# Optimization experiments

Measured on AMD Instinct MI355X. Metric: run time of the kernel, lower is better.

## Reference

```python
import jax, jax.numpy as jnp
import numpy as np

D_MODEL = 1024
N_HEADS = 16
D_KV = 64
B, S = 2, 2048


def setup_inputs() -> dict:
    key = jax.random.key(0)
    ks = jax.random.split(key, 7)
    scale = 1.0 / np.sqrt(D_MODEL)
    return {
        "query": jax.random.normal(ks[0], (B, S, D_MODEL), jnp.float32),
        "key": jax.random.normal(ks[1], (B, S, D_MODEL), jnp.float32),
        "value": jax.random.normal(ks[2], (B, S, D_MODEL), jnp.float32),
        "mask": jnp.zeros((B, 1, 1, S), jnp.float32),
        "Wq": jax.random.normal(ks[3], (D_MODEL, N_HEADS * D_KV), jnp.float32) * scale,
        "Wk": jax.random.normal(ks[4], (D_MODEL, N_HEADS * D_KV), jnp.float32) * scale,
        "Wv": jax.random.normal(ks[5], (D_MODEL, N_HEADS * D_KV), jnp.float32) * scale,
        "Wo": jax.random.normal(ks[6], (N_HEADS * D_KV, D_MODEL), jnp.float32) * scale,
    }


def _split_heads(x):
    b, s, _ = x.shape
    return x.reshape(b, s, N_HEADS, D_KV).transpose(0, 2, 1, 3)  # [B,H,S,Dk]


def reference(query, key, value, mask, Wq, Wk, Wv, Wo):
    q = _split_heads(query @ Wq)
    k = _split_heads(key @ Wk)
    v = _split_heads(value @ Wv)
    scores = jnp.einsum("bhqd,bhkd->bhqk", q, k) / jnp.sqrt(
        jnp.asarray(D_KV, scores_dtype := q.dtype)
    )
    scores = scores + mask
    attn = jax.nn.softmax(scores, axis=-1)  # dropout_rate=0 -> identity
    ctx = jnp.einsum("bhqk,bhkd->bhqd", attn, v)
    ctx = ctx.transpose(0, 2, 1, 3).reshape(query.shape[0], -1, N_HEADS * D_KV)
    hidden = ctx @ Wo
    return hidden
```

## Files before the change

kernel.cpp:

```cpp
#include <hip/hip_runtime.h>
#include <hip/hip_bf16.h>
#include <stdint.h>

typedef __bf16 bf16;
typedef __bf16 bf16x8 __attribute__((ext_vector_type(8)));
typedef __bf16 bf16x4 __attribute__((ext_vector_type(4)));
typedef float  f32x4  __attribute__((ext_vector_type(4)));
typedef float  f32x16 __attribute__((ext_vector_type(16)));

#define S_LEN  2048
#define NH     16
#define DKV    64
#define DMODEL 1024
#define LOG2E  1.4426950408889634f

__device__ __forceinline__ void async_load16(const void* g, void* l) {
  __builtin_amdgcn_global_load_lds(
      (const __attribute__((address_space(1))) uint32_t*)(uintptr_t)g,
      (__attribute__((address_space(3))) uint32_t*)(uintptr_t)l,
      16, 0, 0);
}

__global__ void transpose_w(const float* __restrict__ W0, const float* __restrict__ W1,
                            const float* __restrict__ W2, const float* __restrict__ W3,
                            bf16* __restrict__ T0, bf16* __restrict__ T1,
                            bf16* __restrict__ T2, bf16* __restrict__ T3)
{
  int z = blockIdx.z;
  const float* W = (z == 0) ? W0 : (z == 1) ? W1 : (z == 2) ? W2 : W3;
  bf16* T = (z == 0) ? T0 : (z == 1) ? T1 : (z == 2) ? T2 : T3;
  __shared__ float tile[32][33];
  int n0 = blockIdx.x * 32, k0 = blockIdx.y * 32;
  int tx = threadIdx.x, ty = threadIdx.y;
  for (int i = 0; i < 32; i += 8)
    tile[ty + i][tx] = W[(size_t)(k0 + ty + i) * DMODEL + n0 + tx];
  __syncthreads();
  for (int i = 0; i < 32; i += 8)
    T[(size_t)(n0 + ty + i) * DMODEL + k0 + tx] = (bf16)tile[tx][ty + i];
}

__global__ __launch_bounds__(256) void gemm_qkv(
    const float* __restrict__ Aq, const float* __restrict__ Ak, const float* __restrict__ Av,
    const bf16* __restrict__ Bq, const bf16* __restrict__ Bk, const bf16* __restrict__ Bv,
    bf16* __restrict__ Cq, bf16* __restrict__ Ck, bf16* __restrict__ Cv)
{
  __shared__ __align__(16) char smem[24576];
  bf16* As = (bf16*)smem;
  bf16* Bs = (bf16*)smem + 64 * 64;
  bf16* Ls = (bf16*)smem;

  const int z = blockIdx.z;
  const float* A = (z == 0) ? Aq : (z == 1) ? Ak : Av;
  const bf16* Bt = (z == 0) ? Bq : (z == 1) ? Bk : Bv;
  bf16* C        = (z == 0) ? Cq : (z == 1) ? Ck : Cv;

  const int m0 = blockIdx.x * 64;
  const int n0 = blockIdx.y * 128;
  const int tid = threadIdx.x;
  const int lane = tid & 63;
  const int wave = tid >> 6;
  const int wm = (wave >> 1) * 32;
  const int wn = (wave & 1) * 64;
  const int row = lane & 15;
  const int quad = lane >> 4;

  f32x4 acc[2][4];
  for (int i = 0; i < 2; ++i)
    for (int j = 0; j < 4; ++j) acc[i][j] = (f32x4){0.f, 0.f, 0.f, 0.f};

  const int arc = tid & 7;
  const int arr = tid >> 3;
  const float* A0p = A + (size_t)(m0 + arr) * DMODEL + arc * 8;
  const float* A1p = A + (size_t)(m0 + 32 + arr) * DMODEL + arc * 8;

  f32x4 av0[2], av1[2];
  av0[0] = *(const f32x4*)(A0p);
  av1[0] = *(const f32x4*)(A0p + 4);
  av0[1] = *(const f32x4*)(A1p);
  av1[1] = *(const f32x4*)(A1p + 4);

  for (int kt = 0; kt < 16; ++kt) {
    const int kk = kt << 6;
    __syncthreads();
    for (int j = 0; j < 4; ++j) {
      int base = j * 256 + wave * 64;
      int idx = base + lane;
      int r = idx >> 3;
      int cc = (idx & 7) ^ (r & 7);
      async_load16(Bt + (size_t)(n0 + r) * DMODEL + kk + cc * 8,
                   (char*)Bs + (size_t)base * 16);
    }
    for (int u = 0; u < 2; ++u) {
      bf16x8 o;
      for (int w = 0; w < 4; ++w) { o[w] = (bf16)av0[u][w]; o[w + 4] = (bf16)av1[u][w]; }
      int r = u * 32 + arr;
      *(bf16x8*)(As + r * 64 + ((arc ^ (r & 7)) << 3)) = o;
    }
    __syncthreads();
    if (kt < 15) {
      const int kn = kk + 64;
      av0[0] = *(const f32x4*)(A0p + kn);
      av1[0] = *(const f32x4*)(A0p + kn + 4);
      av0[1] = *(const f32x4*)(A1p + kn);
      av1[1] = *(const f32x4*)(A1p + kn + 4);
    }
    for (int ks = 0; ks < 2; ++ks) {
      bf16x8 af[2], bfr[4];
      for (int i = 0; i < 2; ++i) {
        int rr = wm + i * 16 + row;
        af[i] = *(const bf16x8*)(As + rr * 64 + (((quad + ks * 4) ^ (rr & 7)) << 3));
      }
      for (int j = 0; j < 4; ++j) {
        int rr = wn + j * 16 + row;
        bfr[j] = *(const bf16x8*)(Bs + rr * 64 + (((quad + ks * 4) ^ (rr & 7)) << 3));
      }
      for (int i = 0; i < 2; ++i)
        for (int j = 0; j < 4; ++j)
          acc[i][j] = __builtin_amdgcn_mfma_f32_16x16x32_bf16(af[i], bfr[j], acc[i][j], 0, 0, 0);
    }
  }

  if (z != 2) {
    const int bq = m0 >> 11;
    __syncthreads();
    for (int i = 0; i < 2; ++i)
      for (int j = 0; j < 4; ++j)
        for (int r = 0; r < 4; ++r)
          Ls[(wm + i * 16 + quad * 4 + r) * 132 + wn + j * 16 + row] = (bf16)acc[i][j][r];
    __syncthreads();
    for (int u = 0; u < 4; ++u) {
      int cc = u * 256 + tid;
      int rloc = cc >> 4, c8 = (cc & 15) * 8;
      int s = (m0 + rloc) & 2047;
      int gn = n0 + c8;
      int h = gn >> 6, d = gn & 63;
      bf16x8 val = *(const bf16x8*)(Ls + rloc * 132 + c8);
      *(bf16x8*)(C + (((size_t)(bq * NH + h)) * S_LEN + s) * DKV + d) = val;
    }
  } else {
    for (int i = 0; i < 2; ++i)
      for (int j = 0; j < 4; ++j) {
        int gm = m0 + wm + i * 16 + quad * 4;
        int gn = n0 + wn + j * 16 + row;
        int b = gm >> 11, s = gm & 2047;
        int h = gn >> 6,  d = gn & 63;
        int bh = b * NH + h;
        int tile = s >> 6, kb = (s & 63) >> 2;
        bf16x4 t;
        for (int r = 0; r < 4; ++r) t[r] = (bf16)acc[i][j][r];
        *(bf16x4*)(C + ((((size_t)bh * 32 + tile) * 16 + kb) * 64 + d) * 4) = t;
      }
  }
}

__global__ __launch_bounds__(256, 4) void attn_kernel(
    const bf16* __restrict__ Qh, const bf16* __restrict__ Kh, const bf16* __restrict__ Vperm,
    const float* __restrict__ mask, bf16* __restrict__ Opart, float* __restrict__ Lpart)
{
  __shared__ __align__(16) bf16 Ks[64 * 64];
  __shared__ __align__(16) bf16 Vts[64 * 64];
  __shared__ __align__(16) float masks2[64];

  const int bh = blockIdx.x;
  const int b = bh >> 4;
  const int q0 = blockIdx.y * 128;
  const int zh = blockIdx.z;
  const int tid = threadIdx.x;
  const int lane = tid & 63;
  const int wave = tid >> 6;
  const int ln = lane & 31;
  const int hi = lane >> 5;
  const float SC2 = 0.125f * LOG2E;

  const int qg = q0 + wave * 32 + ln;
  bf16x8 qf[4];
  {
    const bf16* qrow = Qh + ((size_t)bh * S_LEN + qg) * DKV;
    for (int c = 0; c < 4; ++c)
      qf[c] = *(const bf16x8*)(qrow + c * 16 + hi * 8);
  }

  f32x16 O[2];
  for (int nb = 0; nb < 2; ++nb)
    for (int i = 0; i < 16; ++i) O[nb][i] = 0.f;
  float lsum = 0.f;

  for (int it = 0; it < 16; ++it) {
    const int kv0 = zh * 1024 + it * 64;
    __syncthreads();
    const bf16* vtile = Vperm + ((size_t)bh * 32 + (kv0 >> 6)) * 4096;
    for (int j = 0; j < 2; ++j) {
      int base = j * 256 + wave * 64;
      int idx = base + lane;
      int r = idx >> 3;
      int cc = (idx & 7) ^ (r & 7);
      async_load16(Kh + ((size_t)bh * S_LEN + kv0 + r) * DKV + cc * 8,
                   (char*)Ks + (size_t)base * 16);
      async_load16(vtile + (size_t)idx * 8,
                   (char*)Vts + (size_t)base * 16);
    }
    if (tid < 64) masks2[tid] = mask[b * S_LEN + kv0 + tid] * LOG2E;
    __syncthreads();

    f32x16 Sm[2];
    for (int i = 0; i < 16; ++i) { Sm[0][i] = 0.f; Sm[1][i] = 0.f; }
    for (int c = 0; c < 4; ++c) {
      bf16x8 k0 = *(const bf16x8*)(Ks + ln * 64        + (((2 * c + hi) ^ (ln & 7)) << 3));
      bf16x8 k1 = *(const bf16x8*)(Ks + (32 + ln) * 64 + (((2 * c + hi) ^ (ln & 7)) << 3));
      Sm[0] = __builtin_amdgcn_mfma_f32_32x32x16_bf16(k0, qf[c], Sm[0], 0, 0, 0);
      Sm[1] = __builtin_amdgcn_mfma_f32_32x32x16_bf16(k1, qf[c], Sm[1], 0, 0, 0);
    }

    for (int cg = 0; cg < 4; ++cg) {
      int mb = cg >> 1, g = cg & 1;
      int koff = 32 * mb + 16 * g + 4 * hi;
      f32x4 mklo = *(const f32x4*)(masks2 + koff);
      f32x4 mkhi = *(const f32x4*)(masks2 + koff + 8);
      bf16x8 ap;
      float ls0 = 0.f;
      for (int u = 0; u < 4; ++u) {
        float p = __builtin_amdgcn_exp2f(Sm[mb][g * 8 + u] * SC2 + mklo[u]);
        ls0 += p; ap[u] = (bf16)p;
      }
      for (int u = 0; u < 4; ++u) {
        float p = __builtin_amdgcn_exp2f(Sm[mb][g * 8 + 4 + u] * SC2 + mkhi[u]);
        ls0 += p; ap[4 + u] = (bf16)p;
      }
      lsum += ls0;
      int kb0 = hi + 4 * g + 8 * mb;
      for (int nb = 0; nb < 2; ++nb) {
        int d = nb * 32 + ln;
        bf16x4 lo = *(const bf16x4*)(Vts + ((size_t)kb0 * 64 + d) * 4);
        bf16x4 hv = *(const bf16x4*)(Vts + ((size_t)(kb0 + 2) * 64 + d) * 4);
        bf16x8 bv;
        for (int u = 0; u < 4; ++u) { bv[u] = lo[u]; bv[u + 4] = hv[u]; }
        O[nb] = __builtin_amdgcn_mfma_f32_32x32x16_bf16(ap, bv, O[nb], 0, 0, 0);
      }
    }
  }

  float lt = lsum + __shfl_xor(lsum, 32, 64);
  if (lane < 32)
    Lpart[((size_t)zh * 32 + bh) * S_LEN + q0 + wave * 32 + ln] = lt;

  bf16* ob = Opart + (((size_t)zh * 32 + bh) * S_LEN) * DKV;
  for (int g = 0; g < 4; ++g)
    for (int nb = 0; nb < 2; ++nb)
      for (int j = 0; j < 4; ++j) {
        int qrow = q0 + wave * 32 + j + 8 * g + 4 * hi;
        ob[(size_t)qrow * DKV + nb * 32 + ln] = (bf16)O[nb][g * 4 + j];
      }
}

__global__ __launch_bounds__(256) void gemm_out(
    const bf16* __restrict__ Opart, const float* __restrict__ Lpart,
    const bf16* __restrict__ Wot, float* __restrict__ Cout)
{
  __shared__ __align__(16) bf16 As[32 * 64];
  __shared__ __align__(16) bf16 Bs[128 * 64];
  __shared__ float rinv[NH * 32];

  const int m0 = blockIdx.x * 32;
  const int n0 = blockIdx.y * 128;
  const int tid = threadIdx.x;
  const int lane = tid & 63;
  const int wave = tid >> 6;
  const int wm = (wave >> 1) * 16;
  const int wn = (wave & 1) * 64;
  const int row = lane & 15;
  const int quad = lane >> 4;
  const int b = m0 >> 11;
  const int s0 = m0 & 2047;

  for (int u = 0; u < 2; ++u) {
    int idx = u * 256 + tid;
    int h = idx >> 5, r = idx & 31;
    float l = Lpart[((size_t)(b * NH + h)) * S_LEN + s0 + r]
            + Lpart[((size_t)(32 + b * NH + h)) * S_LEN + s0 + r];
    rinv[idx] = 1.0f / l;
  }

  f32x4 acc[4];
  for (int j = 0; j < 4; ++j) acc[j] = (f32x4){0.f, 0.f, 0.f, 0.f};

  const int arc = tid & 7;
  const int arr = tid >> 3;
  const bf16* O0p = Opart + ((size_t)(b * NH) * S_LEN + s0 + arr) * DKV + arc * 8;
  const bf16* O1p = Opart + ((size_t)(32 + b * NH) * S_LEN + s0 + arr) * DKV + arc * 8;
  const size_t HSTEP = (size_t)S_LEN * DKV;

  bf16x8 h0 = *(const bf16x8*)(O0p);
  bf16x8 h1 = *(const bf16x8*)(O1p);

  for (int kt = 0; kt < 16; ++kt) {
    __syncthreads();
    for (int j = 0; j < 4; ++j) {
      int base = j * 256 + wave * 64;
      int idx = base + lane;
      int r = idx >> 3;
      int cc = (idx & 7) ^ (r & 7);
      async_load16(Wot + (size_t)(n0 + r) * DMODEL + kt * 64 + cc * 8,
                   (char*)Bs + (size_t)base * 16);
    }
    {
      float rv = rinv[kt * 32 + arr];
      bf16x8 o;
      for (int w = 0; w < 8; ++w)
        o[w] = (bf16)(((float)h0[w] + (float)h1[w]) * rv);
      *(bf16x8*)(As + arr * 64 + ((arc ^ (arr & 7)) << 3)) = o;
    }
    __syncthreads();
    if (kt < 15) {
      h0 = *(const bf16x8*)(O0p + (size_t)(kt + 1) * HSTEP);
      h1 = *(const bf16x8*)(O1p + (size_t)(kt + 1) * HSTEP);
    }
    for (int ks = 0; ks < 2; ++ks) {
      bf16x8 af, bfr[4];
      {
        int rr = wm + row;
        af = *(const bf16x8*)(As + rr * 64 + (((quad + ks * 4) ^ (rr & 7)) << 3));
      }
      for (int j = 0; j < 4; ++j) {
        int rr = wn + j * 16 + row;
        bfr[j] = *(const bf16x8*)(Bs + rr * 64 + (((quad + ks * 4) ^ (rr & 7)) << 3));
      }
      for (int j = 0; j < 4; ++j)
        acc[j] = __builtin_amdgcn_mfma_f32_16x16x32_bf16(af, bfr[j], acc[j], 0, 0, 0);
    }
  }

  for (int j = 0; j < 4; ++j)
    for (int r = 0; r < 4; ++r) {
      int gm = m0 + wm + quad * 4 + r;
      int gn = n0 + wn + j * 16 + row;
      Cout[(size_t)gm * DMODEL + gn] = acc[j][r];
    }
}

extern "C" void kernel_launch(void* const* d_in, const int* in_sizes, int n_in,
                              void* d_out, int out_size, void* d_ws, size_t ws_size,
                              hipStream_t stream)
{
  const float* query = (const float*)d_in[0];
  const float* key_  = (const float*)d_in[1];
  const float* value = (const float*)d_in[2];
  const float* mask  = (const float*)d_in[3];
  const float* Wq = (const float*)d_in[4];
  const float* Wk = (const float*)d_in[5];
  const float* Wv = (const float*)d_in[6];
  const float* Wo = (const float*)d_in[7];

  char* ws = (char*)d_ws;
  const size_t MB = (size_t)1 << 20;
  bf16* qh    = (bf16*)(ws + 0 * MB);
  bf16* kh    = (bf16*)(ws + 8 * MB);
  bf16* vperm = (bf16*)(ws + 16 * MB);
  bf16* wot   = (bf16*)(ws + 24 * MB);
  bf16* Opart = (bf16*)(ws + 26 * MB);
  bf16* wqt   = (bf16*)(ws + 26 * MB);
  bf16* wkt   = (bf16*)(ws + 28 * MB);
  bf16* wvt   = (bf16*)(ws + 30 * MB);
  float* Lpart = (float*)(ws + 58 * MB);

  transpose_w<<<dim3(32, 32, 4), dim3(32, 8), 0, stream>>>(Wq, Wk, Wv, Wo, wqt, wkt, wvt, wot);
  gemm_qkv<<<dim3(64, 8, 3), 256, 0, stream>>>(query, key_, value, wqt, wkt, wvt,
                                               qh, kh, vperm);
  attn_kernel<<<dim3(32, 16, 2), 256, 0, stream>>>(qh, kh, vperm, mask, Opart, Lpart);
  gemm_out<<<dim3(128, 8), 256, 0, stream>>>(Opart, Lpart, wot, (float*)d_out);
}
```

Before: 224.4 us.

## Double-buffer LDS tiles with async prefetch in QKV, attention and output kernels

Adds a second LDS buffer for the async-loaded B/K/V tiles in all three main kernels and issues the next tile's global-to-LDS loads before computing on the current one. The __syncthreads pairs are replaced with manual s_waitcnt vmcnt counts, sched_barrier fences and raw s_barrier. The aim is to hide global load latency behind MFMA work. In exchange the kernels use more LDS, which may lower occupancy in the attention kernel, and correctness now depends on hand-counted vmcnt values matching the number of outstanding loads.

Measured after the change: 215.5 us. -4.0%, faster.

```diff
diff --git a/kernel.cpp b/kernel.cpp
--- a/kernel.cpp
+++ b/kernel.cpp
@@ -13,6 +13,11 @@
 #define DKV    64
 #define DMODEL 1024
 #define LOG2E  1.4426950408889634f
+
+#define SBAR()       __builtin_amdgcn_s_barrier()
+#define SFENCE()     __builtin_amdgcn_sched_barrier(0)
+#define WAIT_VM(N)   asm volatile("s_waitcnt vmcnt(" #N ")" ::: "memory")
+#define WAIT_LGKM0() asm volatile("s_waitcnt lgkmcnt(0)" ::: "memory")
 
 __device__ __forceinline__ void async_load16(const void* g, void* l) {
   __builtin_amdgcn_global_load_lds(
@@ -44,10 +49,11 @@
     const bf16* __restrict__ Bq, const bf16* __restrict__ Bk, const bf16* __restrict__ Bv,
     bf16* __restrict__ Cq, bf16* __restrict__ Ck, bf16* __restrict__ Cv)
 {
-  __shared__ __align__(16) char smem[24576];
-  bf16* As = (bf16*)smem;
-  bf16* Bs = (bf16*)smem + 64 * 64;
-  bf16* Ls = (bf16*)smem;
+  __shared__ __align__(16) char smem[40960];
+  bf16* As  = (bf16*)smem;
+  bf16* Bs0 = (bf16*)(smem + 8192);
+  bf16* Bs1 = (bf16*)(smem + 8192 + 16384);
+  bf16* Ls  = (bf16*)smem;
 
   const int z = blockIdx.z;
   const float* A = (z == 0) ? Aq : (z == 1) ? Ak : Av;
@@ -73,37 +79,49 @@
   const float* A0p = A + (size_t)(m0 + arr) * DMODEL + arc * 8;
   const float* A1p = A + (size_t)(m0 + 32 + arr) * DMODEL + arc * 8;
 
-  f32x4 av0[2], av1[2];
-  av0[0] = *(const f32x4*)(A0p);
-  av1[0] = *(const f32x4*)(A0p + 4);
-  av0[1] = *(const f32x4*)(A1p);
-  av1[1] = *(const f32x4*)(A1p + 4);
-
-  for (int kt = 0; kt < 16; ++kt) {
+  auto stageB = [&](int kt, bf16* Bsel) {
     const int kk = kt << 6;
-    __syncthreads();
     for (int j = 0; j < 4; ++j) {
       int base = j * 256 + wave * 64;
       int idx = base + lane;
       int r = idx >> 3;
       int cc = (idx & 7) ^ (r & 7);
       async_load16(Bt + (size_t)(n0 + r) * DMODEL + kk + cc * 8,
-                   (char*)Bs + (size_t)base * 16);
-    }
+                   (char*)Bsel + (size_t)base * 16);
+    }
+  };
+
+  f32x4 av0[2], av1[2];
+  av0[0] = *(const f32x4*)(A0p);
+  av1[0] = *(const f32x4*)(A0p + 4);
+  av0[1] = *(const f32x4*)(A1p);
+  av1[1] = *(const f32x4*)(A1p + 4);
+
+  stageB(0, Bs0);
+
+  for (int kt = 0; kt < 16; ++kt) {
+    bf16* Bcur = (kt & 1) ? Bs1 : Bs0;
+    bf16* Bnxt = (kt & 1) ? Bs0 : Bs1;
+    if (kt < 15) stageB(kt + 1, Bnxt);
     for (int u = 0; u < 2; ++u) {
       bf16x8 o;
       for (int w = 0; w < 4; ++w) { o[w] = (bf16)av0[u][w]; o[w + 4] = (bf16)av1[u][w]; }
       int r = u * 32 + arr;
       *(bf16x8*)(As + r * 64 + ((arc ^ (r & 7)) << 3)) = o;
     }
-    __syncthreads();
     if (kt < 15) {
-      const int kn = kk + 64;
+      const int kn = (kt + 1) << 6;
       av0[0] = *(const f32x4*)(A0p + kn);
       av1[0] = *(const f32x4*)(A0p + kn + 4);
       av0[1] = *(const f32x4*)(A1p + kn);
       av1[1] = *(const f32x4*)(A1p + kn + 4);
     }
+    SFENCE();
+    if (kt < 15) { WAIT_VM(8); }
+    else         { WAIT_VM(0); }
+    WAIT_LGKM0();
+    SBAR();
+    SFENCE();
     for (int ks = 0; ks < 2; ++ks) {
       bf16x8 af[2], bfr[4];
       for (int i = 0; i < 2; ++i) {
@@ -112,12 +130,14 @@
       }
       for (int j = 0; j < 4; ++j) {
         int rr = wn + j * 16 + row;
-        bfr[j] = *(const bf16x8*)(Bs + rr * 64 + (((quad + ks * 4) ^ (rr & 7)) << 3));
+        bfr[j] = *(const bf16x8*)(Bcur + rr * 64 + (((quad + ks * 4) ^ (rr & 7)) << 3));
       }
       for (int i = 0; i < 2; ++i)
         for (int j = 0; j < 4; ++j)
           acc[i][j] = __builtin_amdgcn_mfma_f32_16x16x32_bf16(af[i], bfr[j], acc[i][j], 0, 0, 0);
     }
+    SFENCE();
+    SBAR();
   }
 
   if (z != 2) {
@@ -157,9 +177,9 @@
     const bf16* __restrict__ Qh, const bf16* __restrict__ Kh, const bf16* __restrict__ Vperm,
     const float* __restrict__ mask, bf16* __restrict__ Opart, float* __restrict__ Lpart)
 {
-  __shared__ __align__(16) bf16 Ks[64 * 64];
-  __shared__ __align__(16) bf16 Vts[64 * 64];
-  __shared__ __align__(16) float masks2[64];
+  __shared__ __align__(16) bf16 Ks[2][64 * 64];
+  __shared__ __align__(16) bf16 Vts[2][64 * 64];
+  __shared__ __align__(16) float masks2[2][64];
 
   const int bh = blockIdx.x;
   const int b = bh >> 4;
@@ -180,14 +200,10 @@
       qf[c] = *(const bf16x8*)(qrow + c * 16 + hi * 8);
   }
 
-  f32x16 O[2];
-  for (int nb = 0; nb < 2; ++nb)
-    for (int i = 0; i < 16; ++i) O[nb][i] = 0.f;
-  float lsum = 0.f;
-
-  for (int it = 0; it < 16; ++it) {
+  auto stage = [&](int it, int buf) {
     const int kv0 = zh * 1024 + it * 64;
-    __syncthreads();
+    float mval = 0.f;
+    if (tid < 64) mval = mask[b * S_LEN + kv0 + tid];
     const bf16* vtile = Vperm + ((size_t)bh * 32 + (kv0 >> 6)) * 4096;
     for (int j = 0; j < 2; ++j) {
       int base = j * 256 + wave * 64;
@@ -195,18 +211,35 @@
       int r = idx >> 3;
       int cc = (idx & 7) ^ (r & 7);
       async_load16(Kh + ((size_t)bh * S_LEN + kv0 + r) * DKV + cc * 8,
-                   (char*)Ks + (size_t)base * 16);
+                   (char*)Ks[buf] + (size_t)base * 16);
       async_load16(vtile + (size_t)idx * 8,
-                   (char*)Vts + (size_t)base * 16);
-    }
-    if (tid < 64) masks2[tid] = mask[b * S_LEN + kv0 + tid] * LOG2E;
-    __syncthreads();
+                   (char*)Vts[buf] + (size_t)base * 16);
+    }
+    if (tid < 64) masks2[buf][tid] = mval * LOG2E;
+  };
+
+  f32x16 O[2];
+  for (int nb = 0; nb < 2; ++nb)
+    for (int i = 0; i < 16; ++i) O[nb][i] = 0.f;
+  float lsum = 0.f;
+
+  stage(0, 0);
+
+  for (int it = 0; it < 16; ++it) {
+    const int cur = it & 1;
+    if (it < 15) stage(it + 1, cur ^ 1);
+    SFENCE();
+    if (it < 15) { WAIT_VM(4); }
+    else         { WAIT_VM(0); }
+    WAIT_LGKM0();
+    SBAR();
+    SFENCE();
 
     f32x16 Sm[2];
     for (int i = 0; i < 16; ++i) { Sm[0][i] = 0.f; Sm[1][i] = 0.f; }
     for (int c = 0; c < 4; ++c) {
-      bf16x8 k0 = *(const bf16x8*)(Ks + ln * 64        + (((2 * c + hi) ^ (ln & 7)) << 3));
-      bf16x8 k1 = *(const bf16x8*)(Ks + (32 + ln) * 64 + (((2 * c + hi) ^ (ln & 7)) << 3));
+      bf16x8 k0 = *(const bf16x8*)(Ks[cur] + ln * 64        + (((2 * c + hi) ^ (ln & 7)) << 3));
+      bf16x8 k1 = *(const bf16x8*)(Ks[cur] + (32 + ln) * 64 + (((2 * c + hi) ^ (ln & 7)) << 3));
       Sm[0] = __builtin_amdgcn_mfma_f32_32x32x16_bf16(k0, qf[c], Sm[0], 0, 0, 0);
       Sm[1] = __builtin_amdgcn_mfma_f32_32x32x16_bf16(k1, qf[c], Sm[1], 0, 0, 0);
     }
@@ -214,8 +247,8 @@
     for (int cg = 0; cg < 4; ++cg) {
       int mb = cg >> 1, g = cg & 1;
       int koff = 32 * mb + 16 * g + 4 * hi;
-      f32x4 mklo = *(const f32x4*)(masks2 + koff);
-      f32x4 mkhi = *(const f32x4*)(masks2 + koff + 8);
+      f32x4 mklo = *(const f32x4*)(&masks2[cur][koff]);
+      f32x4 mkhi = *(const f32x4*)(&masks2[cur][koff + 8]);
       bf16x8 ap;
       float ls0 = 0.f;
       for (int u = 0; u < 4; ++u) {
@@ -230,13 +263,15 @@
       int kb0 = hi + 4 * g + 8 * mb;
       for (int nb = 0; nb < 2; ++nb) {
         int d = nb * 32 + ln;
-        bf16x4 lo = *(const bf16x4*)(Vts + ((size_t)kb0 * 64 + d) * 4);
-        bf16x4 hv = *(const bf16x4*)(Vts + ((size_t)(kb0 + 2) * 64 + d) * 4);
+        bf16x4 lo = *(const bf16x4*)(Vts[cur] + ((size_t)kb0 * 64 + d) * 4);
+        bf16x4 hv = *(const bf16x4*)(Vts[cur] + ((size_t)(kb0 + 2) * 64 + d) * 4);
         bf16x8 bv;
         for (int u = 0; u < 4; ++u) { bv[u] = lo[u]; bv[u + 4] = hv[u]; }
         O[nb] = __builtin_amdgcn_mfma_f32_32x32x16_bf16(ap, bv, O[nb], 0, 0, 0);
       }
     }
+    SFENCE();
+    SBAR();
   }
 
   float lt = lsum + __shfl_xor(lsum, 32, 64);
@@ -257,7 +292,7 @@
     const bf16* __restrict__ Wot, float* __restrict__ Cout)
 {
   __shared__ __align__(16) bf16 As[32 * 64];
-  __shared__ __align__(16) bf16 Bs[128 * 64];
+  __shared__ __align__(16) bf16 Bs[2][128 * 64];
   __shared__ float rinv[NH * 32];
 
   const int m0 = blockIdx.x * 32;
@@ -289,19 +324,26 @@
   const bf16* O1p = Opart + ((size_t)(32 + b * NH) * S_LEN + s0 + arr) * DKV + arc * 8;
   const size_t HSTEP = (size_t)S_LEN * DKV;
 
-  bf16x8 h0 = *(const bf16x8*)(O0p);
-  bf16x8 h1 = *(const bf16x8*)(O1p);
-
-  for (int kt = 0; kt < 16; ++kt) {
-    __syncthreads();
+  auto stageB = [&](int kt, int buf) {
     for (int j = 0; j < 4; ++j) {
       int base = j * 256 + wave * 64;
       int idx = base + lane;
       int r = idx >> 3;
       int cc = (idx & 7) ^ (r & 7);
       async_load16(Wot + (size_t)(n0 + r) * DMODEL + kt * 64 + cc * 8,
-                   (char*)Bs + (size_t)base * 16);
-    }
+                   (char*)Bs[buf] + (size_t)base * 16);
+    }
+  };
+
+  stageB(0, 0);
+  bf16x8 h0 = *(const bf16x8*)(O0p);
+  bf16x8 h1 = *(const bf16x8*)(O1p);
+  WAIT_LGKM0();
+  SBAR();
+
+  for (int kt = 0; kt < 16; ++kt) {
+    const int cur = kt & 1;
+    if (kt < 15) stageB(kt + 1, cur ^ 1);
     {
       float rv = rinv[kt * 32 + arr];
       bf16x8 o;
@@ -309,11 +351,16 @@
         o[w] = (bf16)(((float)h0[w] + (float)h1[w]) * rv);
       *(bf16x8*)(As + arr * 64 + ((arc ^ (arr & 7)) << 3)) = o;
     }
-    __syncthreads();
     if (kt < 15) {
       h0 = *(const bf16x8*)(O0p + (size_t)(kt + 1) * HSTEP);
       h1 = *(const bf16x8*)(O1p + (size_t)(kt + 1) * HSTEP);
     }
+    SFENCE();
+    if (kt < 15) { WAIT_VM(6); }
+    else         { WAIT_VM(0); }
+    WAIT_LGKM0();
+    SBAR();
+    SFENCE();
     for (int ks = 0; ks < 2; ++ks) {
       bf16x8 af, bfr[4];
       {
@@ -322,11 +369,13 @@
       }
       for (int j = 0; j < 4; ++j) {
         int rr = wn + j * 16 + row;
-        bfr[j] = *(const bf16x8*)(Bs + rr * 64 + (((quad + ks * 4) ^ (rr & 7)) << 3));
+        bfr[j] = *(const bf16x8*)(Bs[cur] + rr * 64 + (((quad + ks * 4) ^ (rr & 7)) << 3));
       }
       for (int j = 0; j < 4; ++j)
         acc[j] = __builtin_amdgcn_mfma_f32_16x16x32_bf16(af, bfr[j], acc[j], 0, 0, 0);
     }
+    SFENCE();
+    SBAR();
   }
 
   for (int j = 0; j < 4; ++j)
```
